# Performance work log

Hardware: AMD Instinct MI355X
Metric: run time of the kernel (lower is better)

The kernel has to match this reference:

```python
import jax, jax.numpy as jnp
import numpy as np

SIZE = 32          # resize target (self.size)
WIN = 11           # SSIM gaussian window
SIGMA = 1.5
THRESH = 0.3       # cal_thresh
C1 = (0.01 * 255.0) ** 2
C2 = (0.03 * 255.0) ** 2


def _gauss_kernel():
    x = jnp.arange(WIN, dtype=jnp.float32) - (WIN - 1) / 2.0
    g = jnp.exp(-(x ** 2) / (2.0 * SIGMA ** 2))
    g = g / g.sum()
    k = jnp.outer(g, g)
    return jnp.tile(k[None, None], (3, 1, 1, 1))  # [3,1,11,11] depthwise


def _dwconv(x, k):
    # x: [N,3,h,w] depthwise gaussian blur, SAME padding (pytorch-ssim style)
    return jax.lax.conv_general_dilated(x, k, (1, 1), 'SAME', feature_group_count=3)


def _crop_resize(img, box, H, W):
    # img [3,H,W], box cxcywh -> [3,SIZE,SIZE]; mimics int() crop + F.interpolate
    # (bilinear, align_corners=False)
    cx, cy, w, h = box[0], box[1], box[2], box[3]
    x0 = jnp.clip(jnp.floor(cx - w / 2), 0.0, W - 1.0)
    x1 = jnp.clip(jnp.floor(cx + w / 2), 0.0, float(W))
    y0 = jnp.clip(jnp.floor(cy - h / 2), 0.0, H - 1.0)
    y1 = jnp.clip(jnp.floor(cy + h / 2), 0.0, float(H))
    wp = jnp.maximum(x1 - x0, 1.0)  # crop width (>=1 to stay well-defined)
    hp = jnp.maximum(y1 - y0, 1.0)
    d = jnp.arange(SIZE, dtype=jnp.float32) + 0.5
    sx = x0 + jnp.clip(d * wp / SIZE - 0.5, 0.0, wp - 1.0)  # source cols
    sy = y0 + jnp.clip(d * hp / SIZE - 0.5, 0.0, hp - 1.0)  # source rows
    ix0 = jnp.floor(sx); iy0 = jnp.floor(sy)
    fx = sx - ix0; fy = sy - iy0
    ix0 = ix0.astype(jnp.int32); iy0 = iy0.astype(jnp.int32)
    ix1 = jnp.minimum(ix0 + 1, (x0 + wp - 1.0).astype(jnp.int32))
    iy1 = jnp.minimum(iy0 + 1, (y0 + hp - 1.0).astype(jnp.int32))

    def gat(iy, ix):
        return img[:, iy[:, None], ix[None, :]]  # [3,SIZE,SIZE]

    return (gat(iy0, ix0) * ((1 - fy)[None, :, None] * (1 - fx)[None, None, :])
            + gat(iy0, ix1) * ((1 - fy)[None, :, None] * fx[None, None, :])
            + gat(iy1, ix0) * (fy[None, :, None] * (1 - fx)[None, None, :])
            + gat(iy1, ix1) * (fy[None, :, None] * fx[None, None, :]))


def _pairwise_iou(gt, pr, eps=1e-16):
    # gt [B,Ng,4], pr [B,Np,4] cxcywh -> iou [B,Ng,Np] (same math as get_two_box_iou)
    g1, g2 = gt[:, :, None, :2], gt[:, :, None, 2:]
    p1, p2 = pr[:, None, :, :2], pr[:, None, :, 2:]
    tl = jnp.maximum(g1 - g2 / 2, p1 - p2 / 2)
    br = jnp.minimum(g1 + g2 / 2, p1 + p2 / 2)
    a_g = jnp.prod(gt[:, :, 2:], -1)[:, :, None]
    a_p = jnp.prod(pr[:, :, 2:], -1)[:, None, :]
    en = jnp.prod((tl < br).astype(gt.dtype), -1)
    a_i = jnp.prod(br - tl, -1) * en
    return a_i / (a_g + a_p - a_i + eps)


def _forward(imgs, gt_boxes, pred_boxes):
    B, C, H, W = imgs.shape
    Ng, Np = gt_boxes.shape[1], pred_boxes.shape[1]
    iou = _pairwise_iou(gt_boxes, pred_boxes)                        # [B,Ng,Np]
    valid = ((iou > THRESH)
             & (pred_boxes[:, None, :, 2] > 2)
             & (pred_boxes[:, None, :, 3] > 2))
    crop = jax.vmap(lambda im, bx: jax.vmap(lambda b: _crop_resize(im, b, H, W))(bx))
    g = crop(imgs, gt_boxes)    # [B,Ng,3,32,32]
    p = crop(imgs, pred_boxes)  # [B,Np,3,32,32]

    k = _gauss_kernel()
    mu_g = _dwconv(g.reshape(B * Ng, 3, SIZE, SIZE), k).reshape(B, Ng, 3, SIZE, SIZE)
    mu_p = _dwconv(p.reshape(B * Np, 3, SIZE, SIZE), k).reshape(B, Np, 3, SIZE, SIZE)
    sig_g = _dwconv((g * g).reshape(B * Ng, 3, SIZE, SIZE), k).reshape(B, Ng, 3, SIZE, SIZE) - mu_g ** 2
    sig_p = _dwconv((p * p).reshape(B * Np, 3, SIZE, SIZE), k).reshape(B, Np, 3, SIZE, SIZE) - mu_p ** 2

    gp = g[:, :, None] * p[:, None, :]                               # [B,Ng,Np,3,32,32]
    mug = mu_g[:, :, None]; mup = mu_p[:, None, :]
    sig_gp = _dwconv(gp.reshape(B * Ng * Np, 3, SIZE, SIZE), k).reshape(B, Ng, Np, 3, SIZE, SIZE) - mug * mup
    ssim_map = ((2 * mug * mup + C1) * (2 * sig_gp + C2)) / ((mug ** 2 + mup ** 2 + C1) * (sig_g[:, :, None] + sig_p[:, None, :] + C2))
    ssim_pair = ssim_map.mean(axis=(-3, -2, -1))                     # [B,Ng,Np]

    l1_pair = (jnp.abs(g[:, :, None] - p[:, None, :]) / 255.0).mean(axis=(-3, -2, -1))

    wv = valid.astype(imgs.dtype)
    cnt = wv.sum()
    mean_valid = lambda x: (x * wv).sum() / jnp.maximum(cnt, 1.0)
    # original: (L1(p/255,g/255) + SSIM_loss(p,g)).mean() over valid pairs
    loss = mean_valid(l1_pair) + (1.0 - mean_valid(ssim_pair))
    return jnp.where(cnt > 0, loss, jnp.zeros((), imgs.dtype))


def setup_inputs() -> dict:
    key = jax.random.key(0)
    k1, k2, k3, k4 = jax.random.split(key, 4)
    B, H, W, Ng, Np = 4, 640, 640, 16, 64
    imgs = jax.random.uniform(k1, (B, 3, H, W), jnp.float32, 0.0, 255.0)
    cxy = jax.random.uniform(k2, (B, Ng, 2), jnp.float32, 64.0, 576.0)
    wh = jax.random.uniform(k3, (B, Ng, 2), jnp.float32, 16.0, 128.0)
    gt_boxes = jnp.concatenate([cxy, wh], -1)
    # preds = jittered copies of GT so many pairs pass the IoU > 0.3 gate
    pred_boxes = jnp.tile(gt_boxes, (1, Np // Ng, 1)) + jax.random.normal(k4, (B, Np, 4), jnp.float32) * 4.0
    return {"imgs": imgs, "gt_boxes": gt_boxes, "pred_boxes": pred_boxes}


def reference(imgs, gt_boxes, pred_boxes):
    return _forward(imgs, gt_boxes, pred_boxes)
```

## Files before the change

### kernel.cpp

```cpp
#include <hip/hip_runtime.h>
#include <math.h>

#define WIN 11
#define HALF 5
#define SZ 32
#define PST 33
#define BB 4
#define NG 16
#define NP 64
#define IH 640
#define IW 640
#define CPIX 1024
#define NPIX 3072
#define NCROP 320
#define NPAIR 4096
#define NSLOT 512
#define SSIM_C1 6.5025f
#define SSIM_C2 58.5225f

#define GW_INIT {0.001028379f, 0.007598757f, 0.036000791f, 0.109360748f, \
                 0.213005174f, 0.266011868f, 0.213005174f, 0.109360748f, \
                 0.036000791f, 0.007598757f, 0.001028379f}

__global__ __launch_bounds__(256) void k_valid(const float* __restrict__ gt,
                                               const float* __restrict__ pr,
                                               int* __restrict__ list,
                                               int* __restrict__ count) {
    int idx = blockIdx.x * 256 + threadIdx.x;
    int b = idx >> 10;
    int r = idx & 1023;
    int gi = r >> 6, pi = r & 63;
    const float* g = gt + (b * NG + gi) * 4;
    const float* p = pr + (b * NP + pi) * 4;
    float gx = g[0], gy = g[1], gw = g[2], gh = g[3];
    float px = p[0], py = p[1], pw = p[2], ph = p[3];
    float tlx = fmaxf(gx - gw * 0.5f, px - pw * 0.5f);
    float tly = fmaxf(gy - gh * 0.5f, py - ph * 0.5f);
    float brx = fminf(gx + gw * 0.5f, px + pw * 0.5f);
    float bry = fminf(gy + gh * 0.5f, py + ph * 0.5f);
    float en = ((tlx < brx) && (tly < bry)) ? 1.f : 0.f;
    float ai = (brx - tlx) * (bry - tly) * en;
    float iou = ai / (gw * gh + pw * ph - ai + 1e-16f);
    if (iou > 0.3f && pw > 2.f && ph > 2.f) {
        int s = atomicAdd(count, 1);
        list[s] = idx;
    }
}

__global__ __launch_bounds__(256) void k_crop(const float* __restrict__ imgs,
                                              const float* __restrict__ gt,
                                              const float* __restrict__ pr,
                                              float* __restrict__ crops,
                                              float* __restrict__ mus,
                                              float* __restrict__ sigs) {
    const int c = blockIdx.x;
    const int crop = blockIdx.y;
    int b;
    const float* box;
    if (crop < BB * NG) {
        b = crop >> 4;
        box = gt + crop * 4;
    } else {
        int id = crop - BB * NG;
        b = id >> 6;
        box = pr + id * 4;
    }

    __shared__ float s_fx[SZ], s_fy[SZ];
    __shared__ int s_ix0[SZ], s_ix1[SZ], s_iy0[SZ], s_iy1[SZ];
    __shared__ float cr[SZ][PST];
    __shared__ float t1[SZ][PST];
    __shared__ float t2[SZ][PST];

    const int t = threadIdx.x;
    if (t < SZ) {
        float cx = box[0], cy = box[1], bw = box[2], bh = box[3];
        float x0 = fminf(fmaxf(floorf(cx - bw * 0.5f), 0.f), (float)(IW - 1));
        float x1 = fminf(fmaxf(floorf(cx + bw * 0.5f), 0.f), (float)IW);
        float y0 = fminf(fmaxf(floorf(cy - bh * 0.5f), 0.f), (float)(IH - 1));
        float y1 = fminf(fmaxf(floorf(cy + bh * 0.5f), 0.f), (float)IH);
        float wp = fmaxf(x1 - x0, 1.f);
        float hp = fmaxf(y1 - y0, 1.f);
        float d = (float)t + 0.5f;
        float sx = x0 + fminf(fmaxf(d * wp * (1.f / 32.f) - 0.5f, 0.f), wp - 1.f);
        float flx = floorf(sx);
        s_ix0[t] = (int)flx;
        s_fx[t] = sx - flx;
        s_ix1[t] = min((int)flx + 1, (int)(x0 + wp - 1.f));
        float sy = y0 + fminf(fmaxf(d * hp * (1.f / 32.f) - 0.5f, 0.f), hp - 1.f);
        float fly = floorf(sy);
        s_iy0[t] = (int)fly;
        s_fy[t] = sy - fly;
        s_iy1[t] = min((int)fly + 1, (int)(y0 + hp - 1.f));
    }
    __syncthreads();

    const float* ic = imgs + ((size_t)b * 3 + c) * IH * IW;
    const int y = t >> 3;
    const int xb = (t & 7) * 4;
    const float fy = s_fy[y];
    const float* r0 = ic + s_iy0[y] * IW;
    const float* r1 = ic + s_iy1[y] * IW;
    float vv[4];
#pragma unroll
    for (int j = 0; j < 4; ++j) {
        int x = xb + j;
        int ix0 = s_ix0[x], ix1 = s_ix1[x];
        float fx = s_fx[x];
        float v00 = r0[ix0], v01 = r0[ix1], v10 = r1[ix0], v11 = r1[ix1];
        float v = v00 * (1.f - fy) * (1.f - fx) + v01 * (1.f - fy) * fx +
                  v10 * fy * (1.f - fx) + v11 * fy * fx;
        vv[j] = v;
        cr[y][x] = v;
    }
    float* dst = crops + (size_t)crop * NPIX + c * CPIX + t * 4;
    *(float4*)dst = make_float4(vv[0], vv[1], vv[2], vv[3]);
    __syncthreads();

    constexpr float GW[WIN] = GW_INIT;
#pragma unroll
    for (int j = 0; j < 4; ++j) {
        int x = xb + j;
        float a1 = 0.f, a2 = 0.f;
#pragma unroll
        for (int k = 0; k < WIN; ++k) {
            int xx = x + k - HALF;
            if (xx >= 0 && xx < SZ) {
                float v = cr[y][xx];
                a1 += GW[k] * v;
                a2 += GW[k] * v * v;
            }
        }
        t1[y][x] = a1;
        t2[y][x] = a2;
    }
    __syncthreads();
    float m[4], s[4];
#pragma unroll
    for (int j = 0; j < 4; ++j) {
        int x = xb + j;
        float a1 = 0.f, a2 = 0.f;
#pragma unroll
        for (int k = 0; k < WIN; ++k) {
            int yy = y + k - HALF;
            if (yy >= 0 && yy < SZ) {
                a1 += GW[k] * t1[yy][x];
                a2 += GW[k] * t2[yy][x];
            }
        }
        m[j] = a1;
        s[j] = a2 - a1 * a1;
    }
    float* mdst = mus + (size_t)crop * NPIX + c * CPIX + t * 4;
    float* sdst = sigs + (size_t)crop * NPIX + c * CPIX + t * 4;
    *(float4*)mdst = make_float4(m[0], m[1], m[2], m[3]);
    *(float4*)sdst = make_float4(s[0], s[1], s[2], s[3]);
}

__global__ __launch_bounds__(256) void k_pair(const int* __restrict__ list,
                                              const int* __restrict__ count,
                                              const float* __restrict__ crops,
                                              const float* __restrict__ mus,
                                              const float* __restrict__ sigs,
                                              float* __restrict__ pairL1,
                                              float* __restrict__ pairSS) {
    const int c = blockIdx.x;
    const int n = *count;
    const int t = threadIdx.x;
    const int y = t >> 3;
    const int xb = (t & 7) * 4;

    __shared__ float gp[SZ][PST];
    __shared__ float tmp[SZ][PST];
    __shared__ float rl[4], rs[4];
    constexpr float GW[WIN] = GW_INIT;

    for (int slot = blockIdx.y; slot < n; slot += NSLOT) {
        const int pair = list[slot];
        const int b = pair >> 10;
        const int r = pair & 1023;
        const int gi = r >> 6, pi = r & 63;
        const size_t goff = (size_t)(b * NG + gi) * NPIX + c * CPIX;
        const size_t poff = (size_t)(BB * NG + b * NP + pi) * NPIX + c * CPIX;

        float4 gv = *(const float4*)(crops + goff + t * 4);
        float4 pv = *(const float4*)(crops + poff + t * 4);
        float4 mg = *(const float4*)(mus + goff + t * 4);
        float4 mp = *(const float4*)(mus + poff + t * 4);
        float4 sg = *(const float4*)(sigs + goff + t * 4);
        float4 sp = *(const float4*)(sigs + poff + t * 4);

        float l1 = fabsf(gv.x - pv.x) + fabsf(gv.y - pv.y) +
                   fabsf(gv.z - pv.z) + fabsf(gv.w - pv.w);
        gp[y][xb + 0] = gv.x * pv.x;
        gp[y][xb + 1] = gv.y * pv.y;
        gp[y][xb + 2] = gv.z * pv.z;
        gp[y][xb + 3] = gv.w * pv.w;
        __syncthreads();

#pragma unroll
        for (int j = 0; j < 4; ++j) {
            int x = xb + j;
            float a = 0.f;
#pragma unroll
            for (int k = 0; k < WIN; ++k) {
                int xx = x + k - HALF;
                if (xx >= 0 && xx < SZ) a += GW[k] * gp[y][xx];
            }
            tmp[y][x] = a;
        }
        __syncthreads();

        float mgv[4] = {mg.x, mg.y, mg.z, mg.w};
        float mpv[4] = {mp.x, mp.y, mp.z, mp.w};
        float sgv[4] = {sg.x, sg.y, sg.z, sg.w};
        float spv[4] = {sp.x, sp.y, sp.z, sp.w};
        float ss = 0.f;
#pragma unroll
        for (int j = 0; j < 4; ++j) {
            int x = xb + j;
            float a = 0.f;
#pragma unroll
            for (int k = 0; k < WIN; ++k) {
                int yy = y + k - HALF;
                if (yy >= 0 && yy < SZ) a += GW[k] * tmp[yy][x];
            }
            float m1 = mgv[j], m2 = mpv[j];
            float sgp = a - m1 * m2;
            float num = (2.f * m1 * m2 + SSIM_C1) * (2.f * sgp + SSIM_C2);
            float den = (m1 * m1 + m2 * m2 + SSIM_C1) * (sgv[j] + spv[j] + SSIM_C2);
            ss += num / den;
        }

#pragma unroll
        for (int off = 32; off > 0; off >>= 1) {
            l1 += __shfl_down(l1, off);
            ss += __shfl_down(ss, off);
        }
        const int wave = t >> 6, lane = t & 63;
        if (lane == 0) { rl[wave] = l1; rs[wave] = ss; }
        __syncthreads();
        if (t == 0) {
            pairL1[slot * 3 + c] = rl[0] + rl[1] + rl[2] + rl[3];
            pairSS[slot * 3 + c] = rs[0] + rs[1] + rs[2] + rs[3];
        }
    }
}

__global__ __launch_bounds__(256) void k_final(const int* __restrict__ count,
                                               const float* __restrict__ pairL1,
                                               const float* __restrict__ pairSS,
                                               float* __restrict__ out) {
    const int n3 = (*count) * 3;
    const int t = threadIdx.x;
    float L = 0.f, S = 0.f;
    for (int i = t; i < n3; i += 256) {
        L += pairL1[i];
        S += pairSS[i];
    }
    __shared__ float rl[4], rs[4];
#pragma unroll
    for (int off = 32; off > 0; off >>= 1) {
        L += __shfl_down(L, off);
        S += __shfl_down(S, off);
    }
    const int wave = t >> 6, lane = t & 63;
    if (lane == 0) { rl[wave] = L; rs[wave] = S; }
    __syncthreads();
    if (t == 0) {
        float cnt = (float)(*count);
        float Lt = (rl[0] + rl[1] + rl[2] + rl[3]) * (1.0f / (255.0f * (float)NPIX));
        float St = (rs[0] + rs[1] + rs[2] + rs[3]) * (1.0f / (float)NPIX);
        float m = fmaxf(cnt, 1.f);
        float loss = Lt / m + 1.f - St / m;
        out[0] = (cnt > 0.f) ? loss : 0.f;
    }
}

extern "C" void kernel_launch(void* const* d_in, const int* in_sizes, int n_in,
                              void* d_out, int out_size, void* d_ws, size_t ws_size,
                              hipStream_t stream) {
    const float* imgs = (const float*)d_in[0];
    const float* gt = (const float*)d_in[1];
    const float* pr = (const float*)d_in[2];

    float* ws = (float*)d_ws;
    float* crops = ws;
    float* mus = crops + (size_t)NCROP * NPIX;
    float* sigs = mus + (size_t)NCROP * NPIX;
    float* pairL1 = sigs + (size_t)NCROP * NPIX;
    float* pairSS = pairL1 + (size_t)NPAIR * 3;
    int* list = (int*)(pairSS + (size_t)NPAIR * 3);
    int* count = list + NPAIR;

    hipMemsetAsync(count, 0, sizeof(int), stream);
    k_valid<<<NPAIR / 256, 256, 0, stream>>>(gt, pr, list, count);
    k_crop<<<dim3(3, NCROP), 256, 0, stream>>>(imgs, gt, pr, crops, mus, sigs);
    k_pair<<<dim3(3, NSLOT), 256, 0, stream>>>(list, count, crops, mus, sigs, pairL1, pairSS);
    k_final<<<1, 256, 0, stream>>>(count, pairL1, pairSS, (float*)d_out);
}
```

Before: 91.41 us.

## Fuse validity into crop kernel, wave-per-task pair kernel with last-block final reduce

Merges the IoU validity pass into the crop kernel as extra blocks and folds the final reduction into the pair kernel using an atomic done-counter, where the last finishing block sums the partials. This cuts the launch count from four to two. The pair kernel now gives each wave one (pair, channel) task with private shared tiles, so no block-level syncs are needed per task, and each lane handles 16 pixels. The trade-offs are higher register pressure, a serial tail reduction in one block, and 34KB of shared memory per block, which may lower occupancy.

```diff
diff --git a/kernel.cpp b/kernel.cpp
--- a/kernel.cpp
+++ b/kernel.cpp
@@ -14,7 +14,7 @@
 #define NPIX 3072
 #define NCROP 320
 #define NPAIR 4096
-#define NSLOT 512
+#define PAIRGRID 384
 #define SSIM_C1 6.5025f
 #define SSIM_C2 58.5225f
 
@@ -22,39 +22,42 @@
                  0.213005174f, 0.266011868f, 0.213005174f, 0.109360748f, \
                  0.036000791f, 0.007598757f, 0.001028379f}
 
-__global__ __launch_bounds__(256) void k_valid(const float* __restrict__ gt,
-                                               const float* __restrict__ pr,
-                                               int* __restrict__ list,
-                                               int* __restrict__ count) {
-    int idx = blockIdx.x * 256 + threadIdx.x;
-    int b = idx >> 10;
-    int r = idx & 1023;
-    int gi = r >> 6, pi = r & 63;
-    const float* g = gt + (b * NG + gi) * 4;
-    const float* p = pr + (b * NP + pi) * 4;
-    float gx = g[0], gy = g[1], gw = g[2], gh = g[3];
-    float px = p[0], py = p[1], pw = p[2], ph = p[3];
-    float tlx = fmaxf(gx - gw * 0.5f, px - pw * 0.5f);
-    float tly = fmaxf(gy - gh * 0.5f, py - ph * 0.5f);
-    float brx = fminf(gx + gw * 0.5f, px + pw * 0.5f);
-    float bry = fminf(gy + gh * 0.5f, py + ph * 0.5f);
-    float en = ((tlx < brx) && (tly < bry)) ? 1.f : 0.f;
-    float ai = (brx - tlx) * (bry - tly) * en;
-    float iou = ai / (gw * gh + pw * ph - ai + 1e-16f);
-    if (iou > 0.3f && pw > 2.f && ph > 2.f) {
-        int s = atomicAdd(count, 1);
-        list[s] = idx;
-    }
-}
-
-__global__ __launch_bounds__(256) void k_crop(const float* __restrict__ imgs,
-                                              const float* __restrict__ gt,
-                                              const float* __restrict__ pr,
-                                              float* __restrict__ crops,
-                                              float* __restrict__ mus,
-                                              float* __restrict__ sigs) {
-    const int c = blockIdx.x;
-    const int crop = blockIdx.y;
+__global__ __launch_bounds__(256) void k_crop_valid(const float* __restrict__ imgs,
+                                                    const float* __restrict__ gt,
+                                                    const float* __restrict__ pr,
+                                                    float* __restrict__ crops,
+                                                    float* __restrict__ mus,
+                                                    float* __restrict__ sigs,
+                                                    int* __restrict__ list,
+                                                    int* __restrict__ count) {
+    const int blk = blockIdx.x;
+    const int t = threadIdx.x;
+
+    if (blk >= 3 * NCROP) {
+        int idx = (blk - 3 * NCROP) * 256 + t;
+        int b = idx >> 10;
+        int r = idx & 1023;
+        int gi = r >> 6, pi = r & 63;
+        const float* g = gt + (b * NG + gi) * 4;
+        const float* p = pr + (b * NP + pi) * 4;
+        float gx = g[0], gy = g[1], gw = g[2], gh = g[3];
+        float px = p[0], py = p[1], pw = p[2], ph = p[3];
+        float tlx = fmaxf(gx - gw * 0.5f, px - pw * 0.5f);
+        float tly = fmaxf(gy - gh * 0.5f, py - ph * 0.5f);
+        float brx = fminf(gx + gw * 0.5f, px + pw * 0.5f);
+        float bry = fminf(gy + gh * 0.5f, py + ph * 0.5f);
+        float en = ((tlx < brx) && (tly < bry)) ? 1.f : 0.f;
+        float ai = (brx - tlx) * (bry - tly) * en;
+        float iou = ai / (gw * gh + pw * ph - ai + 1e-16f);
+        if (iou > 0.3f && pw > 2.f && ph > 2.f) {
+            int s = atomicAdd(count, 1);
+            list[s] = idx;
+        }
+        return;
+    }
+
+    const int crop = blk / 3;
+    const int c = blk - crop * 3;
     int b;
     const float* box;
     if (crop < BB * NG) {
@@ -72,7 +75,6 @@
     __shared__ float t1[SZ][PST];
     __shared__ float t2[SZ][PST];
 
-    const int t = threadIdx.x;
     if (t < SZ) {
         float cx = box[0], cy = box[1], bw = box[2], bh = box[3];
         float x0 = fminf(fmaxf(floorf(cx - bw * 0.5f), 0.f), (float)(IW - 1));
@@ -163,72 +165,86 @@
                                               const float* __restrict__ mus,
                                               const float* __restrict__ sigs,
                                               float* __restrict__ pairL1,
-                                              float* __restrict__ pairSS) {
-    const int c = blockIdx.x;
+                                              float* __restrict__ pairSS,
+                                              int* __restrict__ done,
+                                              float* __restrict__ out) {
     const int n = *count;
+    const int ntask = n * 3;
     const int t = threadIdx.x;
-    const int y = t >> 3;
-    const int xb = (t & 7) * 4;
-
-    __shared__ float gp[SZ][PST];
-    __shared__ float tmp[SZ][PST];
-    __shared__ float rl[4], rs[4];
+    const int wave = t >> 6, lane = t & 63;
+    const int y = lane >> 1;
+    const int xb = (lane & 1) * 16;
+
+    __shared__ float gp[4][SZ][PST];
+    __shared__ float tp[4][SZ][PST];
+    __shared__ bool s_last;
+    float (*GP)[PST] = gp[wave];
+    float (*TMP)[PST] = tp[wave];
     constexpr float GW[WIN] = GW_INIT;
 
-    for (int slot = blockIdx.y; slot < n; slot += NSLOT) {
+    for (int task = blockIdx.x * 4 + wave; task < ntask; task += gridDim.x * 4) {
+        const int slot = task / 3;
+        const int c = task - slot * 3;
         const int pair = list[slot];
         const int b = pair >> 10;
         const int r = pair & 1023;
         const int gi = r >> 6, pi = r & 63;
-        const size_t goff = (size_t)(b * NG + gi) * NPIX + c * CPIX;
-        const size_t poff = (size_t)(BB * NG + b * NP + pi) * NPIX + c * CPIX;
-
-        float4 gv = *(const float4*)(crops + goff + t * 4);
-        float4 pv = *(const float4*)(crops + poff + t * 4);
-        float4 mg = *(const float4*)(mus + goff + t * 4);
-        float4 mp = *(const float4*)(mus + poff + t * 4);
-        float4 sg = *(const float4*)(sigs + goff + t * 4);
-        float4 sp = *(const float4*)(sigs + poff + t * 4);
-
-        float l1 = fabsf(gv.x - pv.x) + fabsf(gv.y - pv.y) +
-                   fabsf(gv.z - pv.z) + fabsf(gv.w - pv.w);
-        gp[y][xb + 0] = gv.x * pv.x;
-        gp[y][xb + 1] = gv.y * pv.y;
-        gp[y][xb + 2] = gv.z * pv.z;
-        gp[y][xb + 3] = gv.w * pv.w;
-        __syncthreads();
-
-#pragma unroll
-        for (int j = 0; j < 4; ++j) {
+        const size_t goff = (size_t)(b * NG + gi) * NPIX + c * CPIX + y * SZ + xb;
+        const size_t poff = (size_t)(BB * NG + b * NP + pi) * NPIX + c * CPIX + y * SZ + xb;
+
+        float gv[16], pv[16];
+#pragma unroll
+        for (int j4 = 0; j4 < 4; ++j4) {
+            float4 a = *(const float4*)(crops + goff + j4 * 4);
+            float4 bq = *(const float4*)(crops + poff + j4 * 4);
+            gv[j4 * 4 + 0] = a.x; gv[j4 * 4 + 1] = a.y; gv[j4 * 4 + 2] = a.z; gv[j4 * 4 + 3] = a.w;
+            pv[j4 * 4 + 0] = bq.x; pv[j4 * 4 + 1] = bq.y; pv[j4 * 4 + 2] = bq.z; pv[j4 * 4 + 3] = bq.w;
+        }
+        float l1 = 0.f;
+#pragma unroll
+        for (int j = 0; j < 16; ++j) {
+            l1 += fabsf(gv[j] - pv[j]);
+            GP[y][xb + j] = gv[j] * pv[j];
+        }
+
+        float m1[16], m2[16], s1[16], s2[16];
+#pragma unroll
+        for (int j4 = 0; j4 < 4; ++j4) {
+            float4 a = *(const float4*)(mus + goff + j4 * 4);
+            float4 bq = *(const float4*)(mus + poff + j4 * 4);
+            float4 cq = *(const float4*)(sigs + goff + j4 * 4);
+            float4 dq = *(const float4*)(sigs + poff + j4 * 4);
+            m1[j4 * 4 + 0] = a.x; m1[j4 * 4 + 1] = a.y; m1[j4 * 4 + 2] = a.z; m1[j4 * 4 + 3] = a.w;
+            m2[j4 * 4 + 0] = bq.x; m2[j4 * 4 + 1] = bq.y; m2[j4 * 4 + 2] = bq.z; m2[j4 * 4 + 3] = bq.w;
+            s1[j4 * 4 + 0] = cq.x; s1[j4 * 4 + 1] = cq.y; s1[j4 * 4 + 2] = cq.z; s1[j4 * 4 + 3] = cq.w;
+            s2[j4 * 4 + 0] = dq.x; s2[j4 * 4 + 1] = dq.y; s2[j4 * 4 + 2] = dq.z; s2[j4 * 4 + 3] = dq.w;
+        }
+
+#pragma unroll
+        for (int j = 0; j < 16; ++j) {
             int x = xb + j;
             float a = 0.f;
 #pragma unroll
             for (int k = 0; k < WIN; ++k) {
                 int xx = x + k - HALF;
-                if (xx >= 0 && xx < SZ) a += GW[k] * gp[y][xx];
+                if (xx >= 0 && xx < SZ) a += GW[k] * GP[y][xx];
             }
-            tmp[y][x] = a;
-        }
-        __syncthreads();
-
-        float mgv[4] = {mg.x, mg.y, mg.z, mg.w};
-        float mpv[4] = {mp.x, mp.y, mp.z, mp.w};
-        float sgv[4] = {sg.x, sg.y, sg.z, sg.w};
-        float spv[4] = {sp.x, sp.y, sp.z, sp.w};
+            TMP[y][x] = a;
+        }
+
         float ss = 0.f;
 #pragma unroll
-        for (int j = 0; j < 4; ++j) {
+        for (int j = 0; j < 16; ++j) {
             int x = xb + j;
             float a = 0.f;
 #pragma unroll
             for (int k = 0; k < WIN; ++k) {
                 int yy = y + k - HALF;
-                if (yy >= 0 && yy < SZ) a += GW[k] * tmp[yy][x];
+                if (yy >= 0 && yy < SZ) a += GW[k] * TMP[yy][x];
             }
-            float m1 = mgv[j], m2 = mpv[j];
-            float sgp = a - m1 * m2;
-            float num = (2.f * m1 * m2 + SSIM_C1) * (2.f * sgp + SSIM_C2);
-            float den = (m1 * m1 + m2 * m2 + SSIM_C1) * (sgv[j] + spv[j] + SSIM_C2);
+            float sgp = a - m1[j] * m2[j];
+            float num = (2.f * m1[j] * m2[j] + SSIM_C1) * (2.f * sgp + SSIM_C2);
+            float den = (m1[j] * m1[j] + m2[j] * m2[j] + SSIM_C1) * (s1[j] + s2[j] + SSIM_C2);
             ss += num / den;
         }
 
@@ -237,24 +253,24 @@
             l1 += __shfl_down(l1, off);
             ss += __shfl_down(ss, off);
         }
-        const int wave = t >> 6, lane = t & 63;
-        if (lane == 0) { rl[wave] = l1; rs[wave] = ss; }
-        __syncthreads();
-        if (t == 0) {
-            pairL1[slot * 3 + c] = rl[0] + rl[1] + rl[2] + rl[3];
-            pairSS[slot * 3 + c] = rs[0] + rs[1] + rs[2] + rs[3];
-        }
-    }
-}
-
-__global__ __launch_bounds__(256) void k_final(const int* __restrict__ count,
-                                               const float* __restrict__ pairL1,
-                                               const float* __restrict__ pairSS,
-                                               float* __restrict__ out) {
-    const int n3 = (*count) * 3;
-    const int t = threadIdx.x;
+        if (lane == 0) {
+            pairL1[task] = l1;
+            pairSS[task] = ss;
+        }
+    }
+
+    __threadfence();
+    __syncthreads();
+    if (t == 0) {
+        int d = atomicAdd(done, 1);
+        s_last = (d == (int)gridDim.x - 1);
+    }
+    __syncthreads();
+    if (!s_last) return;
+    __threadfence();
+
     float L = 0.f, S = 0.f;
-    for (int i = t; i < n3; i += 256) {
+    for (int i = t; i < ntask; i += 256) {
         L += pairL1[i];
         S += pairSS[i];
     }
@@ -264,11 +280,10 @@
         L += __shfl_down(L, off);
         S += __shfl_down(S, off);
     }
-    const int wave = t >> 6, lane = t & 63;
     if (lane == 0) { rl[wave] = L; rs[wave] = S; }
     __syncthreads();
     if (t == 0) {
-        float cnt = (float)(*count);
+        float cnt = (float)n;
         float Lt = (rl[0] + rl[1] + rl[2] + rl[3]) * (1.0f / (255.0f * (float)NPIX));
         float St = (rs[0] + rs[1] + rs[2] + rs[3]) * (1.0f / (float)NPIX);
         float m = fmaxf(cnt, 1.f);
@@ -292,10 +307,11 @@
     float* pairSS = pairL1 + (size_t)NPAIR * 3;
     int* list = (int*)(pairSS + (size_t)NPAIR * 3);
     int* count = list + NPAIR;
-
-    hipMemsetAsync(count, 0, sizeof(int), stream);
-    k_valid<<<NPAIR / 256, 256, 0, stream>>>(gt, pr, list, count);
-    k_crop<<<dim3(3, NCROP), 256, 0, stream>>>(imgs, gt, pr, crops, mus, sigs);
-    k_pair<<<dim3(3, NSLOT), 256, 0, stream>>>(list, count, crops, mus, sigs, pairL1, pairSS);
-    k_final<<<1, 256, 0, stream>>>(count, pairL1, pairSS, (float*)d_out);
+    int* done = count + 1;
+
+    hipMemsetAsync(count, 0, 2 * sizeof(int), stream);
+    k_crop_valid<<<3 * NCROP + NPAIR / 256, 256, 0, stream>>>(imgs, gt, pr, crops, mus, sigs,
+                                                             list, count);
+    k_pair<<<PAIRGRID, 256, 0, stream>>>(list, count, crops, mus, sigs,
+                                         pairL1, pairSS, done, (float*)d_out);
 }
```

After: 115.8 us. +26.7%, slower.

## Fuse validity check into crop kernel and final reduction into pair kernel

Applied to the files above, without the earlier changes.

Merges the IoU validity kernel into the crop/blur kernel as extra blocks, and folds the final reduction into the pair kernel using a last-block-done atomic counter with thread fences. This cuts the launch count from four kernels to two and removes the launch gaps between them. In exchange, the pair kernel gains a global atomic and fences at its tail, and the done counter must be zeroed by the memset on every call.

```diff
diff --git a/kernel.cpp b/kernel.cpp
--- a/kernel.cpp
+++ b/kernel.cpp
@@ -22,39 +22,42 @@
                  0.213005174f, 0.266011868f, 0.213005174f, 0.109360748f, \
                  0.036000791f, 0.007598757f, 0.001028379f}
 
-__global__ __launch_bounds__(256) void k_valid(const float* __restrict__ gt,
-                                               const float* __restrict__ pr,
-                                               int* __restrict__ list,
-                                               int* __restrict__ count) {
-    int idx = blockIdx.x * 256 + threadIdx.x;
-    int b = idx >> 10;
-    int r = idx & 1023;
-    int gi = r >> 6, pi = r & 63;
-    const float* g = gt + (b * NG + gi) * 4;
-    const float* p = pr + (b * NP + pi) * 4;
-    float gx = g[0], gy = g[1], gw = g[2], gh = g[3];
-    float px = p[0], py = p[1], pw = p[2], ph = p[3];
-    float tlx = fmaxf(gx - gw * 0.5f, px - pw * 0.5f);
-    float tly = fmaxf(gy - gh * 0.5f, py - ph * 0.5f);
-    float brx = fminf(gx + gw * 0.5f, px + pw * 0.5f);
-    float bry = fminf(gy + gh * 0.5f, py + ph * 0.5f);
-    float en = ((tlx < brx) && (tly < bry)) ? 1.f : 0.f;
-    float ai = (brx - tlx) * (bry - tly) * en;
-    float iou = ai / (gw * gh + pw * ph - ai + 1e-16f);
-    if (iou > 0.3f && pw > 2.f && ph > 2.f) {
-        int s = atomicAdd(count, 1);
-        list[s] = idx;
-    }
-}
-
-__global__ __launch_bounds__(256) void k_crop(const float* __restrict__ imgs,
-                                              const float* __restrict__ gt,
-                                              const float* __restrict__ pr,
-                                              float* __restrict__ crops,
-                                              float* __restrict__ mus,
-                                              float* __restrict__ sigs) {
-    const int c = blockIdx.x;
-    const int crop = blockIdx.y;
+__global__ __launch_bounds__(256) void k_crop_valid(const float* __restrict__ imgs,
+                                                    const float* __restrict__ gt,
+                                                    const float* __restrict__ pr,
+                                                    float* __restrict__ crops,
+                                                    float* __restrict__ mus,
+                                                    float* __restrict__ sigs,
+                                                    int* __restrict__ list,
+                                                    int* __restrict__ count) {
+    const int blk = blockIdx.x;
+    const int t = threadIdx.x;
+
+    if (blk >= 3 * NCROP) {
+        int idx = (blk - 3 * NCROP) * 256 + t;
+        int b = idx >> 10;
+        int r = idx & 1023;
+        int gi = r >> 6, pi = r & 63;
+        const float* g = gt + (b * NG + gi) * 4;
+        const float* p = pr + (b * NP + pi) * 4;
+        float gx = g[0], gy = g[1], gw = g[2], gh = g[3];
+        float px = p[0], py = p[1], pw = p[2], ph = p[3];
+        float tlx = fmaxf(gx - gw * 0.5f, px - pw * 0.5f);
+        float tly = fmaxf(gy - gh * 0.5f, py - ph * 0.5f);
+        float brx = fminf(gx + gw * 0.5f, px + pw * 0.5f);
+        float bry = fminf(gy + gh * 0.5f, py + ph * 0.5f);
+        float en = ((tlx < brx) && (tly < bry)) ? 1.f : 0.f;
+        float ai = (brx - tlx) * (bry - tly) * en;
+        float iou = ai / (gw * gh + pw * ph - ai + 1e-16f);
+        if (iou > 0.3f && pw > 2.f && ph > 2.f) {
+            int s = atomicAdd(count, 1);
+            list[s] = idx;
+        }
+        return;
+    }
+
+    const int crop = blk / 3;
+    const int c = blk - crop * 3;
     int b;
     const float* box;
     if (crop < BB * NG) {
@@ -72,7 +75,6 @@
     __shared__ float t1[SZ][PST];
     __shared__ float t2[SZ][PST];
 
-    const int t = threadIdx.x;
     if (t < SZ) {
         float cx = box[0], cy = box[1], bw = box[2], bh = box[3];
         float x0 = fminf(fmaxf(floorf(cx - bw * 0.5f), 0.f), (float)(IW - 1));
@@ -163,16 +165,20 @@
                                               const float* __restrict__ mus,
                                               const float* __restrict__ sigs,
                                               float* __restrict__ pairL1,
-                                              float* __restrict__ pairSS) {
+                                              float* __restrict__ pairSS,
+                                              int* __restrict__ done,
+                                              float* __restrict__ out) {
     const int c = blockIdx.x;
     const int n = *count;
     const int t = threadIdx.x;
     const int y = t >> 3;
     const int xb = (t & 7) * 4;
+    const int wave = t >> 6, lane = t & 63;
 
     __shared__ float gp[SZ][PST];
     __shared__ float tmp[SZ][PST];
     __shared__ float rl[4], rs[4];
+    __shared__ bool s_last;
     constexpr float GW[WIN] = GW_INIT;
 
     for (int slot = blockIdx.y; slot < n; slot += NSLOT) {
@@ -237,7 +243,6 @@
             l1 += __shfl_down(l1, off);
             ss += __shfl_down(ss, off);
         }
-        const int wave = t >> 6, lane = t & 63;
         if (lane == 0) { rl[wave] = l1; rs[wave] = ss; }
         __syncthreads();
         if (t == 0) {
@@ -245,30 +250,32 @@
             pairSS[slot * 3 + c] = rs[0] + rs[1] + rs[2] + rs[3];
         }
     }
-}
-
-__global__ __launch_bounds__(256) void k_final(const int* __restrict__ count,
-                                               const float* __restrict__ pairL1,
-                                               const float* __restrict__ pairSS,
-                                               float* __restrict__ out) {
-    const int n3 = (*count) * 3;
-    const int t = threadIdx.x;
+
+    __threadfence();
+    __syncthreads();
+    if (t == 0) {
+        int d = atomicAdd(done, 1);
+        s_last = (d == (int)(gridDim.x * gridDim.y) - 1);
+    }
+    __syncthreads();
+    if (!s_last) return;
+    __threadfence();
+
+    const int ntask = n * 3;
     float L = 0.f, S = 0.f;
-    for (int i = t; i < n3; i += 256) {
+    for (int i = t; i < ntask; i += 256) {
         L += pairL1[i];
         S += pairSS[i];
     }
-    __shared__ float rl[4], rs[4];
 #pragma unroll
     for (int off = 32; off > 0; off >>= 1) {
         L += __shfl_down(L, off);
         S += __shfl_down(S, off);
     }
-    const int wave = t >> 6, lane = t & 63;
     if (lane == 0) { rl[wave] = L; rs[wave] = S; }
     __syncthreads();
     if (t == 0) {
-        float cnt = (float)(*count);
+        float cnt = (float)n;
         float Lt = (rl[0] + rl[1] + rl[2] + rl[3]) * (1.0f / (255.0f * (float)NPIX));
         float St = (rs[0] + rs[1] + rs[2] + rs[3]) * (1.0f / (float)NPIX);
         float m = fmaxf(cnt, 1.f);
@@ -292,10 +299,11 @@
     float* pairSS = pairL1 + (size_t)NPAIR * 3;
     int* list = (int*)(pairSS + (size_t)NPAIR * 3);
     int* count = list + NPAIR;
-
-    hipMemsetAsync(count, 0, sizeof(int), stream);
-    k_valid<<<NPAIR / 256, 256, 0, stream>>>(gt, pr, list, count);
-    k_crop<<<dim3(3, NCROP), 256, 0, stream>>>(imgs, gt, pr, crops, mus, sigs);
-    k_pair<<<dim3(3, NSLOT), 256, 0, stream>>>(list, count, crops, mus, sigs, pairL1, pairSS);
-    k_final<<<1, 256, 0, stream>>>(count, pairL1, pairSS, (float*)d_out);
+    int* done = count + 1;
+
+    hipMemsetAsync(count, 0, 2 * sizeof(int), stream);
+    k_crop_valid<<<3 * NCROP + NPAIR / 256, 256, 0, stream>>>(imgs, gt, pr, crops, mus, sigs,
+                                                             list, count);
+    k_pair<<<dim3(3, NSLOT), 256, 0, stream>>>(list, count, crops, mus, sigs,
+                                               pairL1, pairSS, done, (float*)d_out);
 }
```

Measured after the change: 199.7 us. 119% more time.

## Fuse IoU validity pass into crop kernel and drop memset launch

Applied to the files above, without the earlier changes.

Merges the pair-validity kernel into the crop kernel as one extra block that uses ballot and prefix counts to write the valid list in deterministic order, so the separate memset and kernel launch go away. The crop blocks now compute their bilinear indices per thread in registers instead of staging them in shared memory behind a barrier. This cuts two launches and a sync, but the single validity block loops serially over all 4096 pairs and may become the tail of the fused kernel.

```diff
diff --git a/kernel.cpp b/kernel.cpp
--- a/kernel.cpp
+++ b/kernel.cpp
@@ -22,39 +22,64 @@
                  0.213005174f, 0.266011868f, 0.213005174f, 0.109360748f, \
                  0.036000791f, 0.007598757f, 0.001028379f}
 
-__global__ __launch_bounds__(256) void k_valid(const float* __restrict__ gt,
-                                               const float* __restrict__ pr,
-                                               int* __restrict__ list,
-                                               int* __restrict__ count) {
-    int idx = blockIdx.x * 256 + threadIdx.x;
-    int b = idx >> 10;
-    int r = idx & 1023;
-    int gi = r >> 6, pi = r & 63;
-    const float* g = gt + (b * NG + gi) * 4;
-    const float* p = pr + (b * NP + pi) * 4;
-    float gx = g[0], gy = g[1], gw = g[2], gh = g[3];
-    float px = p[0], py = p[1], pw = p[2], ph = p[3];
-    float tlx = fmaxf(gx - gw * 0.5f, px - pw * 0.5f);
-    float tly = fmaxf(gy - gh * 0.5f, py - ph * 0.5f);
-    float brx = fminf(gx + gw * 0.5f, px + pw * 0.5f);
-    float bry = fminf(gy + gh * 0.5f, py + ph * 0.5f);
-    float en = ((tlx < brx) && (tly < bry)) ? 1.f : 0.f;
-    float ai = (brx - tlx) * (bry - tly) * en;
-    float iou = ai / (gw * gh + pw * ph - ai + 1e-16f);
-    if (iou > 0.3f && pw > 2.f && ph > 2.f) {
-        int s = atomicAdd(count, 1);
-        list[s] = idx;
-    }
-}
-
-__global__ __launch_bounds__(256) void k_crop(const float* __restrict__ imgs,
-                                              const float* __restrict__ gt,
-                                              const float* __restrict__ pr,
-                                              float* __restrict__ crops,
-                                              float* __restrict__ mus,
-                                              float* __restrict__ sigs) {
-    const int c = blockIdx.x;
-    const int crop = blockIdx.y;
+
+__global__ __launch_bounds__(256) void k_crop_valid(const float* __restrict__ imgs,
+                                                    const float* __restrict__ gt,
+                                                    const float* __restrict__ pr,
+                                                    float* __restrict__ crops,
+                                                    float* __restrict__ mus,
+                                                    float* __restrict__ sigs,
+                                                    int* __restrict__ list,
+                                                    int* __restrict__ count) {
+    const int blk = blockIdx.x;
+    const int t = threadIdx.x;
+
+    if (blk == 3 * NCROP) {
+        __shared__ int s_wcnt[4];
+        __shared__ int s_base;
+        const int wave = t >> 6, lane = t & 63;
+        if (t == 0) s_base = 0;
+#pragma unroll 1
+        for (int iter = 0; iter < NPAIR / 256; ++iter) {
+            int idx = iter * 256 + t;
+            int b = idx >> 10;
+            int r = idx & 1023;
+            int gi = r >> 6, pi = r & 63;
+            const float* g = gt + (b * NG + gi) * 4;
+            const float* p = pr + (b * NP + pi) * 4;
+            float gx = g[0], gy = g[1], gw = g[2], gh = g[3];
+            float px = p[0], py = p[1], pw = p[2], ph = p[3];
+            float tlx = fmaxf(gx - gw * 0.5f, px - pw * 0.5f);
+            float tly = fmaxf(gy - gh * 0.5f, py - ph * 0.5f);
+            float brx = fminf(gx + gw * 0.5f, px + pw * 0.5f);
+            float bry = fminf(gy + gh * 0.5f, py + ph * 0.5f);
+            float en = ((tlx < brx) && (tly < bry)) ? 1.f : 0.f;
+            float ai = (brx - tlx) * (bry - tly) * en;
+            float iou = ai / (gw * gh + pw * ph - ai + 1e-16f);
+            bool valid = (iou > 0.3f && pw > 2.f && ph > 2.f);
+            unsigned long long m = __ballot(valid);
+            if (lane == 0) s_wcnt[wave] = __popcll(m);
+            __syncthreads();
+            int base = s_base;
+            int woff = base;
+#pragma unroll
+            for (int w = 0; w < 4; ++w)
+                if (w < wave) woff += s_wcnt[w];
+            int sum = s_wcnt[0] + s_wcnt[1] + s_wcnt[2] + s_wcnt[3];
+            if (valid) {
+                int pos = woff + __popcll(m & ((1ull << lane) - 1ull));
+                list[pos] = idx;
+            }
+            __syncthreads();
+            if (t == 0) s_base = base + sum;
+        }
+        __syncthreads();
+        if (t == 0) *count = s_base;
+        return;
+    }
+
+    const int crop = blk / 3;
+    const int c = blk - crop * 3;
     int b;
     const float* box;
     if (crop < BB * NG) {
@@ -66,47 +91,41 @@
         box = pr + id * 4;
     }
 
-    __shared__ float s_fx[SZ], s_fy[SZ];
-    __shared__ int s_ix0[SZ], s_ix1[SZ], s_iy0[SZ], s_iy1[SZ];
     __shared__ float cr[SZ][PST];
     __shared__ float t1[SZ][PST];
     __shared__ float t2[SZ][PST];
 
-    const int t = threadIdx.x;
-    if (t < SZ) {
-        float cx = box[0], cy = box[1], bw = box[2], bh = box[3];
-        float x0 = fminf(fmaxf(floorf(cx - bw * 0.5f), 0.f), (float)(IW - 1));
-        float x1 = fminf(fmaxf(floorf(cx + bw * 0.5f), 0.f), (float)IW);
-        float y0 = fminf(fmaxf(floorf(cy - bh * 0.5f), 0.f), (float)(IH - 1));
-        float y1 = fminf(fmaxf(floorf(cy + bh * 0.5f), 0.f), (float)IH);
-        float wp = fmaxf(x1 - x0, 1.f);
-        float hp = fmaxf(y1 - y0, 1.f);
-        float d = (float)t + 0.5f;
-        float sx = x0 + fminf(fmaxf(d * wp * (1.f / 32.f) - 0.5f, 0.f), wp - 1.f);
-        float flx = floorf(sx);
-        s_ix0[t] = (int)flx;
-        s_fx[t] = sx - flx;
-        s_ix1[t] = min((int)flx + 1, (int)(x0 + wp - 1.f));
-        float sy = y0 + fminf(fmaxf(d * hp * (1.f / 32.f) - 0.5f, 0.f), hp - 1.f);
-        float fly = floorf(sy);
-        s_iy0[t] = (int)fly;
-        s_fy[t] = sy - fly;
-        s_iy1[t] = min((int)fly + 1, (int)(y0 + hp - 1.f));
-    }
-    __syncthreads();
-
-    const float* ic = imgs + ((size_t)b * 3 + c) * IH * IW;
+    float cx = box[0], cy = box[1], bw = box[2], bh = box[3];
+    float x0 = fminf(fmaxf(floorf(cx - bw * 0.5f), 0.f), (float)(IW - 1));
+    float x1 = fminf(fmaxf(floorf(cx + bw * 0.5f), 0.f), (float)IW);
+    float y0 = fminf(fmaxf(floorf(cy - bh * 0.5f), 0.f), (float)(IH - 1));
+    float y1 = fminf(fmaxf(floorf(cy + bh * 0.5f), 0.f), (float)IH);
+    float wp = fmaxf(x1 - x0, 1.f);
+    float hp = fmaxf(y1 - y0, 1.f);
+    int xmax = (int)(x0 + wp - 1.f);
+    int ymax = (int)(y0 + hp - 1.f);
+
     const int y = t >> 3;
     const int xb = (t & 7) * 4;
-    const float fy = s_fy[y];
-    const float* r0 = ic + s_iy0[y] * IW;
-    const float* r1 = ic + s_iy1[y] * IW;
+
+    float sy = y0 + fminf(fmaxf(((float)y + 0.5f) * hp * (1.f / 32.f) - 0.5f, 0.f), hp - 1.f);
+    float fly = floorf(sy);
+    int iy0 = (int)fly;
+    float fy = sy - fly;
+    int iy1 = min(iy0 + 1, ymax);
+
+    const float* ic = imgs + ((size_t)b * 3 + c) * IH * IW;
+    const float* r0 = ic + iy0 * IW;
+    const float* r1 = ic + iy1 * IW;
     float vv[4];
 #pragma unroll
     for (int j = 0; j < 4; ++j) {
         int x = xb + j;
-        int ix0 = s_ix0[x], ix1 = s_ix1[x];
-        float fx = s_fx[x];
+        float sx = x0 + fminf(fmaxf(((float)x + 0.5f) * wp * (1.f / 32.f) - 0.5f, 0.f), wp - 1.f);
+        float flx = floorf(sx);
+        int ix0 = (int)flx;
+        float fx = sx - flx;
+        int ix1 = min(ix0 + 1, xmax);
         float v00 = r0[ix0], v01 = r0[ix1], v10 = r1[ix0], v11 = r1[ix1];
         float v = v00 * (1.f - fy) * (1.f - fx) + v01 * (1.f - fy) * fx +
                   v10 * fy * (1.f - fx) + v11 * fy * fx;
@@ -169,6 +188,7 @@
     const int t = threadIdx.x;
     const int y = t >> 3;
     const int xb = (t & 7) * 4;
+    const int wave = t >> 6, lane = t & 63;
 
     __shared__ float gp[SZ][PST];
     __shared__ float tmp[SZ][PST];
@@ -237,7 +257,6 @@
             l1 += __shfl_down(l1, off);
             ss += __shfl_down(ss, off);
         }
-        const int wave = t >> 6, lane = t & 63;
         if (lane == 0) { rl[wave] = l1; rs[wave] = ss; }
         __syncthreads();
         if (t == 0) {
@@ -293,9 +312,9 @@
     int* list = (int*)(pairSS + (size_t)NPAIR * 3);
     int* count = list + NPAIR;
 
-    hipMemsetAsync(count, 0, sizeof(int), stream);
-    k_valid<<<NPAIR / 256, 256, 0, stream>>>(gt, pr, list, count);
-    k_crop<<<dim3(3, NCROP), 256, 0, stream>>>(imgs, gt, pr, crops, mus, sigs);
-    k_pair<<<dim3(3, NSLOT), 256, 0, stream>>>(list, count, crops, mus, sigs, pairL1, pairSS);
+    k_crop_valid<<<3 * NCROP + 1, 256, 0, stream>>>(imgs, gt, pr, crops, mus, sigs,
+                                                    list, count);
+    k_pair<<<dim3(3, NSLOT), 256, 0, stream>>>(list, count, crops, mus, sigs,
+                                               pairL1, pairSS);
     k_final<<<1, 256, 0, stream>>>(count, pairL1, pairSS, (float*)d_out);
 }
```

After: 88.45 us. 1.03x faster.
